# Performance work log

Measured on AMD Instinct MI355X. Metric: run time of the kernel, lower is better.

## Reference

```python
import jax, jax.numpy as jnp
import numpy as np

B, F, O, S, D = 32, 32, 64, 64, 512
LOSS_WEIGHT = 100.0
EPS = 1e-12  # matches the 1e-12 in the focal term


def _l2_normalize(x):
    # torch F.normalize(dim=-1): x / max(||x||, 1e-12)
    n = jnp.linalg.norm(x, axis=-1, keepdims=True)
    return x / jnp.maximum(n, 1e-12)


def setup_inputs() -> dict:
    key = jax.random.key(0)
    k1, k2, k3 = jax.random.split(key, 3)
    pred_obj_features = jax.random.normal(k1, (B, F, O, D), dtype=jnp.float32)
    slot_features = jax.random.normal(k2, (B, F, S, D), dtype=jnp.float32)
    # labels in {-1, 0..O-1}; -1 == ignore_index (unmatched slot)
    pid_labels = jax.random.randint(k3, (F, B, S), 0, O + 1) - 1
    # guarantee at least one non-ignored slot per (f,b) so nll_loss mean is well-defined
    pid_labels = pid_labels.at[..., 0].set(0)
    valid_mask = jnp.ones((F, B), dtype=jnp.bool_)  # `if matched_idx[f]` and `str(b) in matched_idx[f]`
    return {
        "pred_obj_features": pred_obj_features,
        "slot_features": slot_features,
        "pid_labels": pid_labels,
        "valid_mask": valid_mask,
    }


def reference(pred_obj_features, slot_features, pid_labels, valid_mask):
    # pred features are clone().detach()'d in the original -> stop_gradient
    pred = _l2_normalize(jax.lax.stop_gradient(pred_obj_features))   # [B,F,O,D]
    slots = _l2_normalize(slot_features)                             # [B,F,S,D]

    # sim_scores per (frame, batch): slot[f,b] @ pred[f,b].T -> [F,B,S,O]
    sim = jnp.einsum("bfsd,bfod->fbso", slots, pred)

    p = jax.nn.softmax(sim, axis=-1)                                 # softmax over objects (dim=1 of [S,O])
    focal = (1.0 - p + EPS) ** 2 * jnp.log(p + EPS)                  # [F,B,S,O]

    safe_t = jnp.maximum(pid_labels, 0)                              # [F,B,S]
    picked = jnp.take_along_axis(focal, safe_t[..., None], axis=-1)[..., 0]  # [F,B,S]
    m = (pid_labels >= 0).astype(focal.dtype)                        # ignore_index=-1 mask
    cnt = jnp.maximum(m.sum(axis=-1), 1.0)                           # [F,B]
    nll = -(picked * m).sum(axis=-1) / cnt                           # nll_loss mean over non-ignored

    v = valid_mask.astype(nll.dtype)                                 # [F,B]
    loss = (LOSS_WEIGHT * nll * v).sum()
    sums = v.sum()
    return jnp.where(sums > 0, loss / (1.0 * F * sums), loss)
```

## Files before the change

kernel.cpp:

```cpp
#include <hip/hip_runtime.h>
#include <hip/hip_bf16.h>

#define BDIM 256
#define NROW 64
#define DDIM 512
#define BK 128
#define NCHUNK 4
#define LDK 136
#define FDIM 32
#define BBATCH 32
#define NBLK (FDIM * BBATCH)

typedef short bf16x8 __attribute__((ext_vector_type(8)));
typedef float f32x4 __attribute__((ext_vector_type(4)));

__device__ __forceinline__ unsigned short f2bf(float f) {
    unsigned int u = __float_as_uint(f);
    u += 0x7FFFu + ((u >> 16) & 1u);
    return (unsigned short)(u >> 16);
}

__global__ __launch_bounds__(BDIM, 4) void pwl_main(
        const float* __restrict__ pred, const float* __restrict__ slots,
        const int* __restrict__ labels, const unsigned char* __restrict__ vmask,
        float* __restrict__ partial) {
    __shared__ __align__(16) unsigned char smem[2 * NROW * LDK * sizeof(unsigned short)];
    unsigned short (*lA)[LDK] = reinterpret_cast<unsigned short(*)[LDK]>(smem);
    unsigned short (*lB)[LDK] = reinterpret_cast<unsigned short(*)[LDK]>(
        smem + NROW * LDK * sizeof(unsigned short));
    float (*simbuf)[65] = reinterpret_cast<float(*)[65]>(smem);

    __shared__ float rnA[NROW], rnB[NROW];
    __shared__ float wsum_f[4], wsum_c[4];

    const int t   = threadIdx.x;
    const int bid = blockIdx.x;
    const int b   = bid >> 5;
    const int f   = bid & 31;
    const float* gA = slots + (size_t)bid * NROW * DDIM;
    const float* gB = pred  + (size_t)bid * NROW * DDIM;

    const int lane = t & 63;
    const int w    = t >> 6;
    const int wr   = (w >> 1) * 32;
    const int wc   = (w & 1) * 32;
    const int lr   = lane & 15;
    const int lk   = (lane >> 4) * 8;
    const int srow = t >> 5;
    const int scol = t & 31;

    f32x4 acc00 = {0,0,0,0}, acc01 = {0,0,0,0}, acc10 = {0,0,0,0}, acc11 = {0,0,0,0};
    float sa[8], sb[8];
#pragma unroll
    for (int i = 0; i < 8; ++i) { sa[i] = 0.f; sb[i] = 0.f; }

    for (int c = 0; c < NCHUNK; ++c) {
        if (c) __syncthreads();
        const int cbase = c * BK;
#pragma unroll
        for (int i = 0; i < 8; ++i) {
            const int row = i * 8 + srow;
            const float4 va = *reinterpret_cast<const float4*>(gA + row * DDIM + cbase + scol * 4);
            const float4 vb = *reinterpret_cast<const float4*>(gB + row * DDIM + cbase + scol * 4);
            sa[i] += va.x*va.x + va.y*va.y + va.z*va.z + va.w*va.w;
            sb[i] += vb.x*vb.x + vb.y*vb.y + vb.z*vb.z + vb.w*vb.w;
            ushort4 ua, ub;
            ua.x = f2bf(va.x); ua.y = f2bf(va.y); ua.z = f2bf(va.z); ua.w = f2bf(va.w);
            ub.x = f2bf(vb.x); ub.y = f2bf(vb.y); ub.z = f2bf(vb.z); ub.w = f2bf(vb.w);
            *reinterpret_cast<ushort4*>(&lA[row][scol * 4]) = ua;
            *reinterpret_cast<ushort4*>(&lB[row][scol * 4]) = ub;
        }
        __syncthreads();
#pragma unroll
        for (int kk = 0; kk < 4; ++kk) {
            const int kb = kk * 32 + lk;
            const bf16x8 a0 = *reinterpret_cast<const bf16x8*>(&lA[wr      + lr][kb]);
            const bf16x8 a1 = *reinterpret_cast<const bf16x8*>(&lA[wr + 16 + lr][kb]);
            const bf16x8 b0 = *reinterpret_cast<const bf16x8*>(&lB[wc      + lr][kb]);
            const bf16x8 b1 = *reinterpret_cast<const bf16x8*>(&lB[wc + 16 + lr][kb]);
            acc00 = __builtin_amdgcn_mfma_f32_16x16x32_bf16(a0, b0, acc00, 0, 0, 0);
            acc01 = __builtin_amdgcn_mfma_f32_16x16x32_bf16(a0, b1, acc01, 0, 0, 0);
            acc10 = __builtin_amdgcn_mfma_f32_16x16x32_bf16(a1, b0, acc10, 0, 0, 0);
            acc11 = __builtin_amdgcn_mfma_f32_16x16x32_bf16(a1, b1, acc11, 0, 0, 0);
        }
    }

#pragma unroll
    for (int i = 0; i < 8; ++i) {
        float x = sa[i], y = sb[i];
#pragma unroll
        for (int m = 1; m <= 16; m <<= 1) { x += __shfl_xor(x, m); y += __shfl_xor(y, m); }
        if ((t & 31) == 0) {
            const int row = i * 8 + srow;
            rnA[row] = 1.f / fmaxf(sqrtf(x), 1e-12f);
            rnB[row] = 1.f / fmaxf(sqrtf(y), 1e-12f);
        }
    }
    __syncthreads();

    {
        const int r0 = wr + (lane >> 4) * 4;
        const int c0 = wc + lr;
#pragma unroll
        for (int j = 0; j < 4; ++j) {
            simbuf[r0 + j     ][c0     ] = acc00[j] * rnA[r0 + j     ] * rnB[c0     ];
            simbuf[r0 + j     ][c0 + 16] = acc01[j] * rnA[r0 + j     ] * rnB[c0 + 16];
            simbuf[r0 + 16 + j][c0     ] = acc10[j] * rnA[r0 + 16 + j] * rnB[c0     ];
            simbuf[r0 + 16 + j][c0 + 16] = acc11[j] * rnA[r0 + 16 + j] * rnB[c0 + 16];
        }
    }
    __syncthreads();

    float contrib = 0.f, ccnt = 0.f;
    {
        const int s = t >> 2;
        const int q = t & 3;
        float v[16];
        float mx = -1e30f;
#pragma unroll
        for (int jj = 0; jj < 16; ++jj) {
            v[jj] = simbuf[s][q * 16 + jj];
            mx = fmaxf(mx, v[jj]);
        }
        mx = fmaxf(mx, __shfl_xor(mx, 1));
        mx = fmaxf(mx, __shfl_xor(mx, 2));
        float se = 0.f;
#pragma unroll
        for (int jj = 0; jj < 16; ++jj) se += __expf(v[jj] - mx);
        se += __shfl_xor(se, 1);
        se += __shfl_xor(se, 2);
        if (q == 0) {
            const int lab = labels[(f * BBATCH + b) * NROW + s];
            if (lab >= 0) {
                const float simt  = simbuf[s][lab];
                const float pt    = __expf(simt - mx) / se;
                const float u     = 1.f - pt + 1e-12f;
                const float focal = u * u * __logf(pt + 1e-12f);
                contrib = focal;
                ccnt    = 1.f;
            }
        }
    }
#pragma unroll
    for (int m = 1; m <= 32; m <<= 1) {
        contrib += __shfl_xor(contrib, m);
        ccnt    += __shfl_xor(ccnt, m);
    }
    if (lane == 0) { wsum_f[w] = contrib; wsum_c[w] = ccnt; }
    __syncthreads();
    if (t == 0) {
        const float rf  = wsum_f[0] + wsum_f[1] + wsum_f[2] + wsum_f[3];
        const float ri  = wsum_c[0] + wsum_c[1] + wsum_c[2] + wsum_c[3];
        const float cnt = fmaxf(ri, 1.f);
        const float nll = -rf / cnt;
        const float vv  = vmask[f * BBATCH + b] ? 1.f : 0.f;
        partial[bid] = 100.f * nll * vv;
    }
}

__global__ __launch_bounds__(BDIM) void pwl_finalize(
        const unsigned char* __restrict__ vmask, const float* __restrict__ partial,
        float* __restrict__ out) {
    __shared__ float sf[4], sv[4];
    const int t = threadIdx.x;
    const float4 p = reinterpret_cast<const float4*>(partial)[t];
    float s = p.x + p.y + p.z + p.w;
    const uchar4 mv = reinterpret_cast<const uchar4*>(vmask)[t];
    float vs = (mv.x ? 1.f : 0.f) + (mv.y ? 1.f : 0.f) + (mv.z ? 1.f : 0.f) + (mv.w ? 1.f : 0.f);
#pragma unroll
    for (int m = 1; m <= 32; m <<= 1) { s += __shfl_xor(s, m); vs += __shfl_xor(vs, m); }
    if ((t & 63) == 0) { sf[t >> 6] = s; sv[t >> 6] = vs; }
    __syncthreads();
    if (t == 0) {
        const float loss = sf[0] + sf[1] + sf[2] + sf[3];
        const float sums = sv[0] + sv[1] + sv[2] + sv[3];
        out[0] = (sums > 0.f) ? loss / (32.0f * sums) : loss;
    }
}

extern "C" void kernel_launch(void* const* d_in, const int* in_sizes, int n_in,
                              void* d_out, int out_size, void* d_ws, size_t ws_size,
                              hipStream_t stream) {
    const float* pred          = (const float*)d_in[0];
    const float* slots         = (const float*)d_in[1];
    const int* labels          = (const int*)d_in[2];
    const unsigned char* vmask = (const unsigned char*)d_in[3];
    float* out     = (float*)d_out;
    float* partial = (float*)d_ws;

    pwl_main<<<dim3(NBLK), dim3(BDIM), 0, stream>>>(pred, slots, labels, vmask, partial);
    pwl_finalize<<<dim3(1), dim3(BDIM), 0, stream>>>(vmask, partial, out);
}
```

Baseline: 49.45 us.

## Double-buffer LDS tiles and prefetch next K-chunk into registers

The K tile shrinks from 128 to 64 columns, giving eight chunks, and the A/B tiles are double-buffered in LDS. Global loads for the next chunk are issued into registers before the MFMA loop on the current chunk, so each iteration needs one barrier instead of two. This aims to hide global memory latency behind the bf16 conversion and the matrix work. LDS use stays about the same (4x64x72 shorts), but smaller chunks mean more loop iterations and barriers, and the prefetch registers add pressure under launch_bounds occupancy 4.

```diff
diff --git a/kernel.cpp b/kernel.cpp
--- a/kernel.cpp
+++ b/kernel.cpp
@@ -4,9 +4,9 @@
 #define BDIM 256
 #define NROW 64
 #define DDIM 512
-#define BK 128
-#define NCHUNK 4
-#define LDK 136
+#define BK 64
+#define NCHUNK 8
+#define LDK 72
 #define FDIM 32
 #define BBATCH 32
 #define NBLK (FDIM * BBATCH)
@@ -20,14 +20,24 @@
     return (unsigned short)(u >> 16);
 }
 
+__device__ __forceinline__ ushort4 pack4(const float4& v) {
+    ushort4 r;
+    r.x = f2bf(v.x); r.y = f2bf(v.y); r.z = f2bf(v.z); r.w = f2bf(v.w);
+    return r;
+}
+
+__device__ __forceinline__ float sumsq4(const float4& v) {
+    return v.x*v.x + v.y*v.y + v.z*v.z + v.w*v.w;
+}
+
 __global__ __launch_bounds__(BDIM, 4) void pwl_main(
         const float* __restrict__ pred, const float* __restrict__ slots,
         const int* __restrict__ labels, const unsigned char* __restrict__ vmask,
         float* __restrict__ partial) {
-    __shared__ __align__(16) unsigned char smem[2 * NROW * LDK * sizeof(unsigned short)];
-    unsigned short (*lA)[LDK] = reinterpret_cast<unsigned short(*)[LDK]>(smem);
-    unsigned short (*lB)[LDK] = reinterpret_cast<unsigned short(*)[LDK]>(
-        smem + NROW * LDK * sizeof(unsigned short));
+    __shared__ __align__(16) unsigned char smem[4 * NROW * LDK * sizeof(unsigned short)];
+    unsigned short (*lA)[NROW][LDK] = reinterpret_cast<unsigned short(*)[NROW][LDK]>(smem);
+    unsigned short (*lB)[NROW][LDK] = reinterpret_cast<unsigned short(*)[NROW][LDK]>(
+        smem + 2 * NROW * LDK * sizeof(unsigned short));
     float (*simbuf)[65] = reinterpret_cast<float(*)[65]>(smem);
 
     __shared__ float rnA[NROW], rnB[NROW];
@@ -46,38 +56,50 @@
     const int wc   = (w & 1) * 32;
     const int lr   = lane & 15;
     const int lk   = (lane >> 4) * 8;
-    const int srow = t >> 5;
-    const int scol = t & 31;
+    const int tr   = t >> 4;
+    const int ts   = t & 15;
 
     f32x4 acc00 = {0,0,0,0}, acc01 = {0,0,0,0}, acc10 = {0,0,0,0}, acc11 = {0,0,0,0};
-    float sa[8], sb[8];
-#pragma unroll
-    for (int i = 0; i < 8; ++i) { sa[i] = 0.f; sb[i] = 0.f; }
-
+    float sqa[4], sqb[4];
+#pragma unroll
+    for (int i = 0; i < 4; ++i) { sqa[i] = 0.f; sqb[i] = 0.f; }
+
+    float4 va[4], vb[4];
+#pragma unroll
+    for (int i = 0; i < 4; ++i) {
+        const int row = i * 16 + tr;
+        va[i] = *reinterpret_cast<const float4*>(gA + (size_t)row * DDIM + ts * 4);
+        vb[i] = *reinterpret_cast<const float4*>(gB + (size_t)row * DDIM + ts * 4);
+    }
+
+#pragma unroll
     for (int c = 0; c < NCHUNK; ++c) {
-        if (c) __syncthreads();
-        const int cbase = c * BK;
-#pragma unroll
-        for (int i = 0; i < 8; ++i) {
-            const int row = i * 8 + srow;
-            const float4 va = *reinterpret_cast<const float4*>(gA + row * DDIM + cbase + scol * 4);
-            const float4 vb = *reinterpret_cast<const float4*>(gB + row * DDIM + cbase + scol * 4);
-            sa[i] += va.x*va.x + va.y*va.y + va.z*va.z + va.w*va.w;
-            sb[i] += vb.x*vb.x + vb.y*vb.y + vb.z*vb.z + vb.w*vb.w;
-            ushort4 ua, ub;
-            ua.x = f2bf(va.x); ua.y = f2bf(va.y); ua.z = f2bf(va.z); ua.w = f2bf(va.w);
-            ub.x = f2bf(vb.x); ub.y = f2bf(vb.y); ub.z = f2bf(vb.z); ub.w = f2bf(vb.w);
-            *reinterpret_cast<ushort4*>(&lA[row][scol * 4]) = ua;
-            *reinterpret_cast<ushort4*>(&lB[row][scol * 4]) = ub;
+        const int p = c & 1;
+#pragma unroll
+        for (int i = 0; i < 4; ++i) {
+            const int row = i * 16 + tr;
+            sqa[i] += sumsq4(va[i]);
+            sqb[i] += sumsq4(vb[i]);
+            *reinterpret_cast<ushort4*>(&lA[p][row][ts * 4]) = pack4(va[i]);
+            *reinterpret_cast<ushort4*>(&lB[p][row][ts * 4]) = pack4(vb[i]);
+        }
+        if (c + 1 < NCHUNK) {
+            const int cb = (c + 1) * BK;
+#pragma unroll
+            for (int i = 0; i < 4; ++i) {
+                const int row = i * 16 + tr;
+                va[i] = *reinterpret_cast<const float4*>(gA + (size_t)row * DDIM + cb + ts * 4);
+                vb[i] = *reinterpret_cast<const float4*>(gB + (size_t)row * DDIM + cb + ts * 4);
+            }
         }
         __syncthreads();
 #pragma unroll
-        for (int kk = 0; kk < 4; ++kk) {
+        for (int kk = 0; kk < 2; ++kk) {
             const int kb = kk * 32 + lk;
-            const bf16x8 a0 = *reinterpret_cast<const bf16x8*>(&lA[wr      + lr][kb]);
-            const bf16x8 a1 = *reinterpret_cast<const bf16x8*>(&lA[wr + 16 + lr][kb]);
-            const bf16x8 b0 = *reinterpret_cast<const bf16x8*>(&lB[wc      + lr][kb]);
-            const bf16x8 b1 = *reinterpret_cast<const bf16x8*>(&lB[wc + 16 + lr][kb]);
+            const bf16x8 a0 = *reinterpret_cast<const bf16x8*>(&lA[p][wr      + lr][kb]);
+            const bf16x8 a1 = *reinterpret_cast<const bf16x8*>(&lA[p][wr + 16 + lr][kb]);
+            const bf16x8 b0 = *reinterpret_cast<const bf16x8*>(&lB[p][wc      + lr][kb]);
+            const bf16x8 b1 = *reinterpret_cast<const bf16x8*>(&lB[p][wc + 16 + lr][kb]);
             acc00 = __builtin_amdgcn_mfma_f32_16x16x32_bf16(a0, b0, acc00, 0, 0, 0);
             acc01 = __builtin_amdgcn_mfma_f32_16x16x32_bf16(a0, b1, acc01, 0, 0, 0);
             acc10 = __builtin_amdgcn_mfma_f32_16x16x32_bf16(a1, b0, acc10, 0, 0, 0);
@@ -86,12 +108,12 @@
     }
 
 #pragma unroll
-    for (int i = 0; i < 8; ++i) {
-        float x = sa[i], y = sb[i];
-#pragma unroll
-        for (int m = 1; m <= 16; m <<= 1) { x += __shfl_xor(x, m); y += __shfl_xor(y, m); }
-        if ((t & 31) == 0) {
-            const int row = i * 8 + srow;
+    for (int i = 0; i < 4; ++i) {
+        float x = sqa[i], y = sqb[i];
+#pragma unroll
+        for (int m = 1; m <= 8; m <<= 1) { x += __shfl_xor(x, m); y += __shfl_xor(y, m); }
+        if (ts == 0) {
+            const int row = i * 16 + tr;
             rnA[row] = 1.f / fmaxf(sqrtf(x), 1e-12f);
             rnB[row] = 1.f / fmaxf(sqrtf(y), 1e-12f);
         }
```

Result: slower. 128.5 us (+159.9%).
